# Performance work log

Measured on AMD Instinct MI355X. Metric: run time of the kernel, lower is better.

Reference implementation:

```python
import jax, jax.numpy as jnp
import numpy as np

EPS = 1e-4  # BatchNorm eps from module


def setup_inputs() -> dict:
    key = jax.random.key(0)
    ks = jax.random.split(key, 7)
    N, C, H, W = 4, 256, 64, 64
    D = C  # reduction=1
    x = jax.random.normal(ks[0], (N, C, H, W), dtype=jnp.float32)
    # 1x1 conv weights, msra-style scaled init
    s = 1.0 / np.sqrt(C)
    Wq = jax.random.normal(ks[1], (D, C), dtype=jnp.float32) * s
    Wk = jax.random.normal(ks[2], (D, C), dtype=jnp.float32) * s
    Wv = jax.random.normal(ks[3], (D, C), dtype=jnp.float32) * s
    Wo = jax.random.normal(ks[4], (C, D), dtype=jnp.float32) * s
    gamma = jnp.ones((C,), dtype=jnp.float32)
    beta = jnp.zeros((C,), dtype=jnp.float32)
    return {"x": x, "Wq": Wq, "Wk": Wk, "Wv": Wv, "Wo": Wo, "gamma": gamma, "beta": beta}


def reference(x, Wq, Wk, Wv, Wo, gamma, beta):
    N, C, H, W = x.shape
    D = Wq.shape[0]
    scale = 1.0 / jnp.sqrt(jnp.float32(D))
    xf = x.reshape(N, C, H * W)                      # (N, C, L)
    # 1x1 convs == per-position linear projections
    q = jnp.einsum('dc,ncl->nld', Wq, xf)            # (N, L, D)
    k = jnp.einsum('dc,ncl->nld', Wk, xf)            # (N, L, D)
    v = jnp.einsum('dc,ncl->nld', Wv, xf)            # (N, L, D)
    scores = jnp.einsum('nld,nmd->nlm', q, k) * scale  # (N, L, L)
    attn = jax.nn.softmax(scores, axis=2)
    out = jnp.einsum('nlm,nmd->nld', attn, v)        # (N, L, D)
    out = jnp.einsum('od,nld->nol', Wo, out).reshape(N, C, H, W)
    # BatchNorm2d (training-mode batch statistics, biased variance)
    mean = jnp.mean(out, axis=(0, 2, 3), keepdims=True)
    var = jnp.var(out, axis=(0, 2, 3), keepdims=True)
    out = (out - mean) * jax.lax.rsqrt(var + EPS)
    out = out * gamma[None, :, None, None] + beta[None, :, None, None]
    return x + out
```

## Files before the change

kernel.cpp:

```cpp
#include <hip/hip_runtime.h>
#include <cstdint>
#include <cstddef>

#define NB 4
#define CH 256
#define LL 4096

typedef unsigned short u16;
typedef unsigned int u32;
typedef unsigned char u8;
typedef __attribute__((ext_vector_type(8))) short bf16x8;
typedef __attribute__((ext_vector_type(4))) float f32x4;

#define GPTR(p) ((const __attribute__((address_space(1))) u32*)(p))
#define LPTR(p) ((__attribute__((address_space(3))) u32*)(p))

__device__ __forceinline__ float blo(u32 x) { return __uint_as_float(x << 16); }
__device__ __forceinline__ float bhi(u32 x) { return __uint_as_float(x & 0xffff0000u); }
__device__ __forceinline__ float b2f(u16 h) { return __uint_as_float(((u32)h) << 16); }
__device__ __forceinline__ u16 f2b(float f) {
    u32 u = __float_as_uint(f);
    u32 r = (u + 0x7fffu + ((u >> 16) & 1u)) >> 16;
    return (u16)r;
}
__device__ __forceinline__ u32 pack2(float a, float b) {
    return (u32)f2b(a) | ((u32)f2b(b) << 16);
}

__global__ __launch_bounds__(256) void castw_kernel(
    const float* __restrict__ Wq, const float* __restrict__ Wk,
    const float* __restrict__ Wv, const float* __restrict__ Wo,
    u16* __restrict__ Wb, float* __restrict__ stats) {
    const int i = blockIdx.x * 256 + threadIdx.x;
    const int m = blockIdx.y;
    if (m == 0 && blockIdx.x < 2) stats[i] = 0.0f;
    const float* src = (m == 0) ? Wq : (m == 1) ? Wk : (m == 2) ? Wv : Wo;
    float4 v = ((const float4*)src)[i];
    uint2 o;
    o.x = pack2(v.x, v.y);
    o.y = pack2(v.z, v.w);
    ((uint2*)(Wb + m * 65536))[i] = o;
}

__global__ __launch_bounds__(256) void tcast_kernel(
    const float* __restrict__ x, u16* __restrict__ xT) {
    const int n = blockIdx.z;
    const int c0 = blockIdx.y * 64, l0 = blockIdx.x * 64;
    __shared__ u16 t[64][72];
    const float* xs = x + (size_t)n * CH * LL;
    const int tid = threadIdx.x;
    const int lq = (tid & 15) * 4, cc = tid >> 4;
#pragma unroll
    for (int p = 0; p < 4; ++p) {
        int c = cc + p * 16;
        float4 v = *(const float4*)&xs[(size_t)(c0 + c) * LL + l0 + lq];
        t[lq + 0][c] = f2b(v.x);
        t[lq + 1][c] = f2b(v.y);
        t[lq + 2][c] = f2b(v.z);
        t[lq + 3][c] = f2b(v.w);
    }
    __syncthreads();
    u16* xo = xT + (size_t)n * LL * CH;
    const int l = tid >> 2, c8 = (tid & 3) * 16;
#pragma unroll
    for (int h = 0; h < 2; ++h) {
        uint4 vv = *(uint4*)&t[l][c8 + h * 8];
        *(uint4*)&xo[(size_t)(l0 + l) * CH + c0 + c8 + h * 8] = vv;
    }
}

__global__ __launch_bounds__(256, 2) void projqk_kernel(
    const u16* __restrict__ xT, const u16* __restrict__ Wb,
    u16* __restrict__ q, u16* __restrict__ k) {
    const int n = blockIdx.z;
    const int dhalf = blockIdx.y & 1, mat = blockIdx.y >> 1;
    const int l0 = blockIdx.x * 64;
    const int d0 = dhalf * 128;
    const int tid = threadIdx.x;
    const int w = tid >> 6, lane = tid & 63;
    const int lhi = lane >> 4, llo = lane & 15;

    __shared__ __align__(16) u16 Bs[128 * 256];

    const u16* xn = xT + (size_t)n * LL * CH;
    const u16* Wm = Wb + mat * 65536 + (size_t)d0 * CH;

#pragma unroll
    for (int i = 0; i < 16; ++i) {
        int s = i * 256 + tid;
        int r = s >> 5, c = s & 31;
        __builtin_amdgcn_global_load_lds(GPTR(Wm + r * CH + (c ^ (r & 31)) * 8),
                                         LPTR((char*)Bs + i * 4096 + w * 1024),
                                         16, 0, 0);
    }

    bf16x8 af[8];
    const u16* abase = xn + (size_t)(l0 + w * 16 + llo) * CH + lhi * 8;
#pragma unroll
    for (int ks = 0; ks < 8; ++ks) af[ks] = *(const bf16x8*)(abase + ks * 32);

    f32x4 acc[8];
#pragma unroll
    for (int t = 0; t < 8; ++t) acc[t] = (f32x4){0.f, 0.f, 0.f, 0.f};

    __syncthreads();

#pragma unroll
    for (int ks = 0; ks < 8; ++ks) {
#pragma unroll
        for (int ct = 0; ct < 8; ++ct) {
            const int rr = ct * 16 + llo;
            bf16x8 bf = *(const bf16x8*)(Bs + rr * CH +
                                         ((ks * 4 + lhi) ^ (rr & 31)) * 8);
            acc[ct] = __builtin_amdgcn_mfma_f32_16x16x32_bf16(af[ks], bf, acc[ct], 0, 0, 0);
        }
    }

    u16* o = (mat ? k : q) + (size_t)n * LL * CH;
#pragma unroll
    for (int r = 0; r < 4; ++r) {
        int lr = l0 + w * 16 + lhi * 4 + r;
#pragma unroll
        for (int ct = 0; ct < 8; ++ct)
            o[(size_t)lr * CH + d0 + ct * 16 + llo] = f2b(acc[ct][r]);
    }
}

__global__ __launch_bounds__(256, 2) void projv_kernel(
    const u16* __restrict__ xT, const u16* __restrict__ Wb,
    u16* __restrict__ vT) {
    const int n = blockIdx.z;
    const int d0 = blockIdx.y * 64;
    const int l0 = blockIdx.x * 128;
    const int tid = threadIdx.x;
    const int w = tid >> 6, lane = tid & 63;
    const int lhi = lane >> 4, llo = lane & 15;

    __shared__ __align__(16) u16 Bs[128 * 256];

    const u16* xn = xT + (size_t)n * LL * CH + (size_t)l0 * CH;
    const u16* Wm = Wb + 2 * 65536;

#pragma unroll
    for (int i = 0; i < 16; ++i) {
        int s = i * 256 + tid;
        int r = s >> 5, c = s & 31;
        __builtin_amdgcn_global_load_lds(GPTR(xn + r * CH + (c ^ (r & 31)) * 8),
                                         LPTR((char*)Bs + i * 4096 + w * 1024),
                                         16, 0, 0);
    }

    bf16x8 af[8];
    const u16* abase = Wm + (size_t)(d0 + w * 16 + llo) * CH + lhi * 8;
#pragma unroll
    for (int ks = 0; ks < 8; ++ks) af[ks] = *(const bf16x8*)(abase + ks * 32);

    f32x4 acc[8];
#pragma unroll
    for (int t = 0; t < 8; ++t) acc[t] = (f32x4){0.f, 0.f, 0.f, 0.f};

    __syncthreads();

#pragma unroll
    for (int ks = 0; ks < 8; ++ks) {
#pragma unroll
        for (int ct = 0; ct < 8; ++ct) {
            const int rr = ct * 16 + llo;
            bf16x8 bf = *(const bf16x8*)(Bs + rr * CH +
                                         ((ks * 4 + lhi) ^ (rr & 31)) * 8);
            acc[ct] = __builtin_amdgcn_mfma_f32_16x16x32_bf16(af[ks], bf, acc[ct], 0, 0, 0);
        }
    }

    u16* o = vT + (size_t)n * CH * LL;
#pragma unroll
    for (int r = 0; r < 4; ++r) {
        int dr = d0 + w * 16 + lhi * 4 + r;
#pragma unroll
        for (int ct = 0; ct < 8; ++ct)
            o[(size_t)dr * LL + l0 + ct * 16 + llo] = f2b(acc[ct][r]);
    }
}

__global__ __launch_bounds__(256, 2) void fattn_kernel(
    const u16* __restrict__ q, const u16* __restrict__ k,
    const u16* __restrict__ vT, u16* __restrict__ Op, float* __restrict__ l_s,
    int iters) {
    const int n = blockIdx.y;
    const int s_id = blockIdx.z;
    const int l0 = blockIdx.x * 128;
    const int m_base = s_id * iters * 32;
    const int tid = threadIdx.x;
    const int w = tid >> 6;
    const int lane = tid & 63;
    const int lhi = lane >> 4, llo = lane & 15;

    __shared__ __align__(16) char smem[65536];

    bf16x8 qf[2][8];
    {
        const u16* base = q + (size_t)(n * LL + l0 + w * 32 + llo) * CH + lhi * 8;
#pragma unroll
        for (int t = 0; t < 2; ++t)
#pragma unroll
            for (int ks = 0; ks < 8; ++ks)
                qf[t][ks] = *(const bf16x8*)(base + t * 16 * CH + ks * 32);
    }

    const u16* kg = k + (size_t)n * LL * CH;
    const u16* vg = vT + (size_t)n * CH * LL;

    int okK[4], okV[4];
#pragma unroll
    for (int i = 0; i < 4; ++i) {
        int s = i * 256 + tid;
        int rK = s >> 5;
        int cK = (s & 31) ^ rK;
        okK[i] = rK * CH + cK * 8;
        int dV = s >> 2;
        int cV = (s & 3) ^ ((dV & 3) ^ ((dV >> 2) & 3));
        okV[i] = dV * LL + cV * 8;
    }

    f32x4 oacc[2][16];
#pragma unroll
    for (int t = 0; t < 2; ++t)
#pragma unroll
        for (int ct = 0; ct < 16; ++ct) oacc[t][ct] = (f32x4){0.f, 0.f, 0.f, 0.f};
    float lrun[2] = {0.f, 0.f};

    const float C1 = 0.09016844005556021f;
    const int posV = (lhi ^ ((llo & 3) ^ (llo >> 2))) * 8;
    const int idxA = (llo + 32 * (lhi & 1)) * 4;
    const int idxB = idxA + 64;
    const bool selLo = (lhi < 2);

    {
        const u16* kg2 = kg + (size_t)m_base * CH;
        const u16* vg2 = vg + m_base;
#pragma unroll
        for (int i = 0; i < 4; ++i) {
            __builtin_amdgcn_global_load_lds(GPTR(kg2 + okK[i]),
                                             LPTR(smem + i * 4096 + w * 1024), 16, 0, 0);
            __builtin_amdgcn_global_load_lds(GPTR(vg2 + okV[i]),
                                             LPTR(smem + 32768 + i * 4096 + w * 1024),
                                             16, 0, 0);
        }
    }

    for (int it = 0; it < iters; ++it) {
        __syncthreads();
        if (it + 1 < iters) {
            const int m1 = m_base + (it + 1) * 32;
            const u16* kg2 = kg + (size_t)m1 * CH;
            const u16* vg2 = vg + m1;
            char* Kb = smem + ((it + 1) & 1) * 16384;
            char* Vb = smem + 32768 + ((it + 1) & 1) * 16384;
#pragma unroll
            for (int i = 0; i < 4; ++i) {
                __builtin_amdgcn_global_load_lds(GPTR(kg2 + okK[i]),
                                                 LPTR(Kb + i * 4096 + w * 1024), 16, 0, 0);
                __builtin_amdgcn_global_load_lds(GPTR(vg2 + okV[i]),
                                                 LPTR(Vb + i * 4096 + w * 1024), 16, 0, 0);
            }
        }
        const u16* Kl = (const u16*)(smem + (it & 1) * 16384);
        const u16* Vl = (const u16*)(smem + 32768 + (it & 1) * 16384);

        f32x4 s00 = (f32x4){0.f, 0.f, 0.f, 0.f};
        f32x4 s01 = (f32x4){0.f, 0.f, 0.f, 0.f};
        f32x4 s10 = (f32x4){0.f, 0.f, 0.f, 0.f};
        f32x4 s11 = (f32x4){0.f, 0.f, 0.f, 0.f};
#pragma unroll
        for (int ks = 0; ks < 8; ++ks) {
            const int cq = ks * 4 + lhi;
            bf16x8 b0 = *(const bf16x8*)(Kl + llo * 256 + (cq ^ llo) * 8);
            bf16x8 b1 = *(const bf16x8*)(Kl + (llo + 16) * 256 + (cq ^ (llo + 16)) * 8);
            s00 = __builtin_amdgcn_mfma_f32_16x16x32_bf16(b0, qf[0][ks], s00, 0, 0, 0);
            s10 = __builtin_amdgcn_mfma_f32_16x16x32_bf16(b0, qf[1][ks], s10, 0, 0, 0);
            s01 = __builtin_amdgcn_mfma_f32_16x16x32_bf16(b1, qf[0][ks], s01, 0, 0, 0);
            s11 = __builtin_amdgcn_mfma_f32_16x16x32_bf16(b1, qf[1][ks], s11, 0, 0, 0);
        }

        bf16x8 pa[2];
#pragma unroll
        for (int qt = 0; qt < 2; ++qt) {
            f32x4 sa = qt ? s10 : s00;
            f32x4 sb = qt ? s11 : s01;
            float pA0 = __builtin_amdgcn_exp2f(sa[0] * C1);
            float pA1 = __builtin_amdgcn_exp2f(sa[1] * C1);
            float pA2 = __builtin_amdgcn_exp2f(sa[2] * C1);
            float pA3 = __builtin_amdgcn_exp2f(sa[3] * C1);
            float pB0 = __builtin_amdgcn_exp2f(sb[0] * C1);
            float pB1 = __builtin_amdgcn_exp2f(sb[1] * C1);
            float pB2 = __builtin_amdgcn_exp2f(sb[2] * C1);
            float pB3 = __builtin_amdgcn_exp2f(sb[3] * C1);
            lrun[qt] += ((pA0 + pA1) + (pA2 + pA3)) + ((pB0 + pB1) + (pB2 + pB3));
            u32 w0, w1, w2, w3;
            asm("v_cvt_pk_bf16_f32 %0, %1, %2" : "=v"(w0) : "v"(pA0), "v"(pA1));
            asm("v_cvt_pk_bf16_f32 %0, %1, %2" : "=v"(w1) : "v"(pA2), "v"(pA3));
            asm("v_cvt_pk_bf16_f32 %0, %1, %2" : "=v"(w2) : "v"(pB0), "v"(pB1));
            asm("v_cvt_pk_bf16_f32 %0, %1, %2" : "=v"(w3) : "v"(pB2), "v"(pB3));
            int t0 = __builtin_amdgcn_ds_bpermute(idxA, (int)w0);
            int t2 = __builtin_amdgcn_ds_bpermute(idxA, (int)w2);
            int u0 = __builtin_amdgcn_ds_bpermute(idxA, (int)w1);
            int u2 = __builtin_amdgcn_ds_bpermute(idxA, (int)w3);
            int v0 = __builtin_amdgcn_ds_bpermute(idxB, (int)w0);
            int v2 = __builtin_amdgcn_ds_bpermute(idxB, (int)w2);
            int x0 = __builtin_amdgcn_ds_bpermute(idxB, (int)w1);
            int x2 = __builtin_amdgcn_ds_bpermute(idxB, (int)w3);
            union { u32 u[4]; bf16x8 v; } pk;
            pk.u[0] = selLo ? (u32)t0 : (u32)t2;
            pk.u[1] = selLo ? (u32)u0 : (u32)u2;
            pk.u[2] = selLo ? (u32)v0 : (u32)v2;
            pk.u[3] = selLo ? (u32)x0 : (u32)x2;
            pa[qt] = pk.v;
        }

#pragma unroll
        for (int ct = 0; ct < 16; ++ct) {
            bf16x8 vf = *(const bf16x8*)(Vl + (ct * 16 + llo) * 32 + posV);
            oacc[0][ct] = __builtin_amdgcn_mfma_f32_16x16x32_bf16(pa[0], vf, oacc[0][ct], 0, 0, 0);
            oacc[1][ct] = __builtin_amdgcn_mfma_f32_16x16x32_bf16(pa[1], vf, oacc[1][ct], 0, 0, 0);
        }
    }

    u16* ap = Op + (size_t)((s_id * NB + n) * (size_t)LL + l0 + w * 32) * CH;
    float* lp = l_s + (size_t)s_id * NB * LL + (size_t)n * LL + l0 + w * 32;
#pragma unroll
    for (int t = 0; t < 2; ++t) {
        float ls = lrun[t];
        ls += __shfl_xor(ls, 16);
        ls += __shfl_xor(ls, 32);
        if (lhi == 0) lp[t * 16 + llo] = ls;
#pragma unroll
        for (int r = 0; r < 4; ++r) {
            int lrow = t * 16 + lhi * 4 + r;
#pragma unroll
            for (int ct = 0; ct < 16; ++ct) {
                ap[(size_t)lrow * CH + ct * 16 + llo] = f2b(oacc[t][ct][r]);
            }
        }
    }
}

__global__ __launch_bounds__(256) void merge_kernel(
    const u16* __restrict__ Op, const float* __restrict__ l_s,
    u16* __restrict__ att, int S) {
    const size_t t8 = (size_t)blockIdx.x * 256 + threadIdx.x;
    const size_t flat = t8 * 8;
    const size_t row = flat >> 8;
    float lsum = 0.0f;
    for (int s = 0; s < S; ++s) lsum += l_s[(size_t)s * NB * LL + row];
    const float inv = 1.0f / lsum;
    float acc[8];
#pragma unroll
    for (int j = 0; j < 8; ++j) acc[j] = 0.0f;
    for (int s = 0; s < S; ++s) {
        uint4 raw = *(const uint4*)(Op + (size_t)s * NB * LL * CH + flat);
        acc[0] += blo(raw.x); acc[1] += bhi(raw.x);
        acc[2] += blo(raw.y); acc[3] += bhi(raw.y);
        acc[4] += blo(raw.z); acc[5] += bhi(raw.z);
        acc[6] += blo(raw.w); acc[7] += bhi(raw.w);
    }
    uint4 o;
    o.x = pack2(acc[0] * inv, acc[1] * inv);
    o.y = pack2(acc[2] * inv, acc[3] * inv);
    o.z = pack2(acc[4] * inv, acc[5] * inv);
    o.w = pack2(acc[6] * inv, acc[7] * inv);
    *(uint4*)(att + flat) = o;
}

__global__ __launch_bounds__(256, 2) void outm_kernel(
    const u16* __restrict__ Wb, const u16* __restrict__ att,
    u16* __restrict__ y, float* __restrict__ stats) {
    const int n = blockIdx.z;
    const int o0 = blockIdx.y * 64;
    const int l0 = blockIdx.x * 128;
    const int tid = threadIdx.x;
    const int w = tid >> 6, lane = tid & 63;
    const int lhi = lane >> 4, llo = lane & 15;

    __shared__ __align__(16) u16 Bs[128 * 256];

    const u16* an = att + (size_t)n * LL * CH + (size_t)l0 * CH;
    const u16* Wm = Wb + 3 * 65536;

#pragma unroll
    for (int i = 0; i < 16; ++i) {
        int s = i * 256 + tid;
        int r = s >> 5, c = s & 31;
        __builtin_amdgcn_global_load_lds(GPTR(an + r * CH + (c ^ (r & 31)) * 8),
                                         LPTR((char*)Bs + i * 4096 + w * 1024),
                                         16, 0, 0);
    }

    bf16x8 af[8];
    const u16* abase = Wm + (size_t)(o0 + w * 16 + llo) * CH + lhi * 8;
#pragma unroll
    for (int ks = 0; ks < 8; ++ks) af[ks] = *(const bf16x8*)(abase + ks * 32);

    f32x4 acc[8];
#pragma unroll
    for (int t = 0; t < 8; ++t) acc[t] = (f32x4){0.f, 0.f, 0.f, 0.f};

    __syncthreads();

#pragma unroll
    for (int ks = 0; ks < 8; ++ks) {
#pragma unroll
        for (int ct = 0; ct < 8; ++ct) {
            const int rr = ct * 16 + llo;
            bf16x8 bf = *(const bf16x8*)(Bs + rr * CH +
                                         ((ks * 4 + lhi) ^ (rr & 31)) * 8);
            acc[ct] = __builtin_amdgcn_mfma_f32_16x16x32_bf16(af[ks], bf, acc[ct], 0, 0, 0);
        }
    }

    u16* yn = y + (size_t)n * CH * LL;
#pragma unroll
    for (int r = 0; r < 4; ++r) {
        const int orow = o0 + w * 16 + lhi * 4 + r;
        float ts = 0.0f, tq = 0.0f;
#pragma unroll
        for (int ct = 0; ct < 8; ++ct) {
            float vv = acc[ct][r];
            yn[(size_t)orow * LL + l0 + ct * 16 + llo] = f2b(vv);
            ts += vv;
            tq += vv * vv;
        }
        ts += __shfl_xor(ts, 1); tq += __shfl_xor(tq, 1);
        ts += __shfl_xor(ts, 2); tq += __shfl_xor(tq, 2);
        ts += __shfl_xor(ts, 4); tq += __shfl_xor(tq, 4);
        ts += __shfl_xor(ts, 8); tq += __shfl_xor(tq, 8);
        if (llo == 0) {
            atomicAdd(&stats[orow], ts);
            atomicAdd(&stats[256 + orow], tq);
        }
    }
}

__global__ __launch_bounds__(256) void bn_kernel(
    const float* __restrict__ x, const u16* __restrict__ y,
    const float* __restrict__ stats, const float* __restrict__ gamma,
    const float* __restrict__ beta, float* __restrict__ out) {
    const int idx = blockIdx.x * 256 + threadIdx.x;
    const int base = idx * 4;
    const int c = (base >> 12) & 255;
    const float cnt = 1.0f / 16384.0f;
    float mean = stats[c] * cnt;
    float var = stats[256 + c] * cnt - mean * mean;
    float rstd = rsqrtf(var + 1e-4f);
    float g = gamma[c] * rstd;
    float b = beta[c];
    uint2 yv = ((const uint2*)y)[idx];
    float4 xv = ((const float4*)x)[idx];
    float4 o;
    o.x = xv.x + (blo(yv.x) - mean) * g + b;
    o.y = xv.y + (bhi(yv.x) - mean) * g + b;
    o.z = xv.z + (blo(yv.y) - mean) * g + b;
    o.w = xv.w + (bhi(yv.y) - mean) * g + b;
    ((float4*)out)[idx] = o;
}

extern "C" void kernel_launch(void* const* d_in, const int* in_sizes, int n_in,
                              void* d_out, int out_size, void* d_ws, size_t ws_size,
                              hipStream_t stream) {
    const float* x = (const float*)d_in[0];
    const float* Wq = (const float*)d_in[1];
    const float* Wk = (const float*)d_in[2];
    const float* Wv = (const float*)d_in[3];
    const float* Wo = (const float*)d_in[4];
    const float* gamma = (const float*)d_in[5];
    const float* beta = (const float*)d_in[6];
    float* out = (float*)d_out;

    const size_t elems = (size_t)NB * LL * CH;

    int S = 1;
    for (int cand = 4; cand >= 2; cand >>= 1) {
        size_t need = elems * 2 * (size_t)(3 + cand) +
                      (size_t)cand * NB * LL * 4 + 524288 + 8192;
        if (ws_size >= need) { S = cand; break; }
    }
    const int iters = 128 / S;

    char* wsb = (char*)d_ws;
    u16* q = (u16*)wsb;
    u16* k = q + elems;
    u16* vT = k + elems;
    u16* Op = vT + elems;
    u16* xT = Op;
    float* l_s = (float*)(Op + (size_t)S * elems);
    u16* Wb = (u16*)(l_s + (size_t)S * NB * LL);
    float* stats = (float*)(Wb + 4 * 65536);
    u16* att = q;
    u16* y = k;

    castw_kernel<<<dim3(64, 4), 256, 0, stream>>>(Wq, Wk, Wv, Wo, Wb, stats);
    tcast_kernel<<<dim3(LL / 64, CH / 64, NB), 256, 0, stream>>>(x, xT);
    projqk_kernel<<<dim3(LL / 64, 4, NB), 256, 0, stream>>>(xT, Wb, q, k);
    projv_kernel<<<dim3(LL / 128, CH / 64, NB), 256, 0, stream>>>(xT, Wb, vT);
    fattn_kernel<<<dim3(LL / 128, NB, S), 256, 0, stream>>>(q, k, vT, Op, l_s, iters);
    merge_kernel<<<(int)(elems / 8 / 256), 256, 0, stream>>>(Op, l_s, att, S);
    outm_kernel<<<dim3(LL / 128, CH / 64, NB), 256, 0, stream>>>(Wb, att, y, stats);
    bn_kernel<<<(NB * CH * LL / 4) / 256, 256, 0, stream>>>(x, y, stats, gamma, beta, out);
}
```

Baseline: 208.6 us.

## Software-pipeline PV matmul one iteration behind QK scores in attention loop

Restructures the attention inner loop so the P·V MFMA accumulation for the previous key block runs after the current block's QK^T scores. The exp/convert/permute of the current block then overlaps with the PV MFMAs. The V tile load now happens in the same iteration it is consumed, one iteration later, and a drained PV step is added after the loop with an extra barrier. This costs extra registers for the carried probabilities and relies on the barrier placement to keep the V double buffer consistent.

```diff
diff --git a/kernel.cpp b/kernel.cpp
--- a/kernel.cpp
+++ b/kernel.cpp
@@ -237,35 +237,36 @@
 
     {
         const u16* kg2 = kg + (size_t)m_base * CH;
-        const u16* vg2 = vg + m_base;
 #pragma unroll
         for (int i = 0; i < 4; ++i) {
             __builtin_amdgcn_global_load_lds(GPTR(kg2 + okK[i]),
                                              LPTR(smem + i * 4096 + w * 1024), 16, 0, 0);
-            __builtin_amdgcn_global_load_lds(GPTR(vg2 + okV[i]),
-                                             LPTR(smem + 32768 + i * 4096 + w * 1024),
-                                             16, 0, 0);
-        }
-    }
+        }
+    }
+
+    bf16x8 paP[2];
 
     for (int it = 0; it < iters; ++it) {
         __syncthreads();
         if (it + 1 < iters) {
-            const int m1 = m_base + (it + 1) * 32;
-            const u16* kg2 = kg + (size_t)m1 * CH;
-            const u16* vg2 = vg + m1;
+            const u16* kg2 = kg + (size_t)(m_base + (it + 1) * 32) * CH;
             char* Kb = smem + ((it + 1) & 1) * 16384;
-            char* Vb = smem + 32768 + ((it + 1) & 1) * 16384;
 #pragma unroll
             for (int i = 0; i < 4; ++i) {
                 __builtin_amdgcn_global_load_lds(GPTR(kg2 + okK[i]),
                                                  LPTR(Kb + i * 4096 + w * 1024), 16, 0, 0);
+            }
+        }
+        {
+            const u16* vg2 = vg + m_base + it * 32;
+            char* Vb = smem + 32768 + (it & 1) * 16384;
+#pragma unroll
+            for (int i = 0; i < 4; ++i) {
                 __builtin_amdgcn_global_load_lds(GPTR(vg2 + okV[i]),
                                                  LPTR(Vb + i * 4096 + w * 1024), 16, 0, 0);
             }
         }
         const u16* Kl = (const u16*)(smem + (it & 1) * 16384);
-        const u16* Vl = (const u16*)(smem + 32768 + (it & 1) * 16384);
 
         f32x4 s00 = (f32x4){0.f, 0.f, 0.f, 0.f};
         f32x4 s01 = (f32x4){0.f, 0.f, 0.f, 0.f};
@@ -282,7 +283,16 @@
             s11 = __builtin_amdgcn_mfma_f32_16x16x32_bf16(b1, qf[1][ks], s11, 0, 0, 0);
         }
 
-        bf16x8 pa[2];
+        if (it > 0) {
+            const u16* Vp = (const u16*)(smem + 32768 + ((it - 1) & 1) * 16384);
+#pragma unroll
+            for (int ct = 0; ct < 16; ++ct) {
+                bf16x8 vf = *(const bf16x8*)(Vp + (ct * 16 + llo) * 32 + posV);
+                oacc[0][ct] = __builtin_amdgcn_mfma_f32_16x16x32_bf16(paP[0], vf, oacc[0][ct], 0, 0, 0);
+                oacc[1][ct] = __builtin_amdgcn_mfma_f32_16x16x32_bf16(paP[1], vf, oacc[1][ct], 0, 0, 0);
+            }
+        }
+
 #pragma unroll
         for (int qt = 0; qt < 2; ++qt) {
             f32x4 sa = qt ? s10 : s00;
@@ -314,14 +324,18 @@
             pk.u[1] = selLo ? (u32)u0 : (u32)u2;
             pk.u[2] = selLo ? (u32)v0 : (u32)v2;
             pk.u[3] = selLo ? (u32)x0 : (u32)x2;
-            pa[qt] = pk.v;
-        }
-
+            paP[qt] = pk.v;
+        }
+    }
+
+    __syncthreads();
+    {
+        const u16* Vp = (const u16*)(smem + 32768 + ((iters - 1) & 1) * 16384);
 #pragma unroll
         for (int ct = 0; ct < 16; ++ct) {
-            bf16x8 vf = *(const bf16x8*)(Vl + (ct * 16 + llo) * 32 + posV);
-            oacc[0][ct] = __builtin_amdgcn_mfma_f32_16x16x32_bf16(pa[0], vf, oacc[0][ct], 0, 0, 0);
-            oacc[1][ct] = __builtin_amdgcn_mfma_f32_16x16x32_bf16(pa[1], vf, oacc[1][ct], 0, 0, 0);
+            bf16x8 vf = *(const bf16x8*)(Vp + (ct * 16 + llo) * 32 + posV);
+            oacc[0][ct] = __builtin_amdgcn_mfma_f32_16x16x32_bf16(paP[0], vf, oacc[0][ct], 0, 0, 0);
+            oacc[1][ct] = __builtin_amdgcn_mfma_f32_16x16x32_bf16(paP[1], vf, oacc[1][ct], 0, 0, 0);
         }
     }
 
```

Measured after the change: 218.8 us. 1.05x slower.

## Single-buffer V in attention for 3 blocks/CU and merge prep/projection launches

Applied to the files above, without the earlier changes.

The attention kernel keeps K double-buffered but holds V in a single shared buffer. The next V tile is loaded after the PV MFMAs, behind a barrier. This cuts LDS from 64 KB to 48 KB and raises launch bounds to 3 blocks per CU, aiming for higher occupancy. The cost is that V load latency is no longer hidden behind compute, and the tighter register budget may cause spills. Separately, the weight cast and x transpose-cast kernels are merged into one launch, and the QK and V projection kernels into another, to cut launch overhead.

```diff
diff --git a/kernel.cpp b/kernel.cpp
--- a/kernel.cpp
+++ b/kernel.cpp
@@ -27,162 +27,161 @@
     return (u32)f2b(a) | ((u32)f2b(b) << 16);
 }
 
-__global__ __launch_bounds__(256) void castw_kernel(
-    const float* __restrict__ Wq, const float* __restrict__ Wk,
-    const float* __restrict__ Wv, const float* __restrict__ Wo,
-    u16* __restrict__ Wb, float* __restrict__ stats) {
-    const int i = blockIdx.x * 256 + threadIdx.x;
-    const int m = blockIdx.y;
-    if (m == 0 && blockIdx.x < 2) stats[i] = 0.0f;
-    const float* src = (m == 0) ? Wq : (m == 1) ? Wk : (m == 2) ? Wv : Wo;
-    float4 v = ((const float4*)src)[i];
-    uint2 o;
-    o.x = pack2(v.x, v.y);
-    o.y = pack2(v.z, v.w);
-    ((uint2*)(Wb + m * 65536))[i] = o;
-}
-
-__global__ __launch_bounds__(256) void tcast_kernel(
-    const float* __restrict__ x, u16* __restrict__ xT) {
-    const int n = blockIdx.z;
-    const int c0 = blockIdx.y * 64, l0 = blockIdx.x * 64;
+__global__ __launch_bounds__(256) void prep_kernel(
+    const float* __restrict__ x, const float* __restrict__ Wq,
+    const float* __restrict__ Wk, const float* __restrict__ Wv,
+    const float* __restrict__ Wo, u16* __restrict__ Wb,
+    float* __restrict__ stats, u16* __restrict__ xT) {
+    const int id = blockIdx.x;
+    const int tid = threadIdx.x;
     __shared__ u16 t[64][72];
-    const float* xs = x + (size_t)n * CH * LL;
-    const int tid = threadIdx.x;
-    const int lq = (tid & 15) * 4, cc = tid >> 4;
-#pragma unroll
-    for (int p = 0; p < 4; ++p) {
-        int c = cc + p * 16;
-        float4 v = *(const float4*)&xs[(size_t)(c0 + c) * LL + l0 + lq];
-        t[lq + 0][c] = f2b(v.x);
-        t[lq + 1][c] = f2b(v.y);
-        t[lq + 2][c] = f2b(v.z);
-        t[lq + 3][c] = f2b(v.w);
-    }
-    __syncthreads();
-    u16* xo = xT + (size_t)n * LL * CH;
-    const int l = tid >> 2, c8 = (tid & 3) * 16;
-#pragma unroll
-    for (int h = 0; h < 2; ++h) {
-        uint4 vv = *(uint4*)&t[l][c8 + h * 8];
-        *(uint4*)&xo[(size_t)(l0 + l) * CH + c0 + c8 + h * 8] = vv;
-    }
-}
-
-__global__ __launch_bounds__(256, 2) void projqk_kernel(
+    if (id < 1024) {
+        const int n = id >> 8;
+        const int c0 = ((id >> 6) & 3) * 64, l0 = (id & 63) * 64;
+        const float* xs = x + (size_t)n * CH * LL;
+        const int lq = (tid & 15) * 4, cc = tid >> 4;
+#pragma unroll
+        for (int p = 0; p < 4; ++p) {
+            int c = cc + p * 16;
+            float4 v = *(const float4*)&xs[(size_t)(c0 + c) * LL + l0 + lq];
+            t[lq + 0][c] = f2b(v.x);
+            t[lq + 1][c] = f2b(v.y);
+            t[lq + 2][c] = f2b(v.z);
+            t[lq + 3][c] = f2b(v.w);
+        }
+        __syncthreads();
+        u16* xo = xT + (size_t)n * LL * CH;
+        const int l = tid >> 2, c8 = (tid & 3) * 16;
+#pragma unroll
+        for (int h = 0; h < 2; ++h) {
+            uint4 vv = *(uint4*)&t[l][c8 + h * 8];
+            *(uint4*)&xo[(size_t)(l0 + l) * CH + c0 + c8 + h * 8] = vv;
+        }
+    } else {
+        const int j = id - 1024;
+        const int i = (j & 63) * 256 + tid;
+        const int m = j >> 6;
+        if (m == 0 && (j & 63) < 2) stats[i] = 0.0f;
+        const float* src = (m == 0) ? Wq : (m == 1) ? Wk : (m == 2) ? Wv : Wo;
+        float4 v = ((const float4*)src)[i];
+        uint2 o;
+        o.x = pack2(v.x, v.y);
+        o.y = pack2(v.z, v.w);
+        ((uint2*)(Wb + m * 65536))[i] = o;
+    }
+}
+
+__global__ __launch_bounds__(256, 2) void proj_kernel(
     const u16* __restrict__ xT, const u16* __restrict__ Wb,
-    u16* __restrict__ q, u16* __restrict__ k) {
-    const int n = blockIdx.z;
-    const int dhalf = blockIdx.y & 1, mat = blockIdx.y >> 1;
-    const int l0 = blockIdx.x * 64;
-    const int d0 = dhalf * 128;
+    u16* __restrict__ q, u16* __restrict__ k, u16* __restrict__ vT) {
+    const int id = blockIdx.x;
     const int tid = threadIdx.x;
     const int w = tid >> 6, lane = tid & 63;
     const int lhi = lane >> 4, llo = lane & 15;
 
     __shared__ __align__(16) u16 Bs[128 * 256];
 
-    const u16* xn = xT + (size_t)n * LL * CH;
-    const u16* Wm = Wb + mat * 65536 + (size_t)d0 * CH;
-
-#pragma unroll
-    for (int i = 0; i < 16; ++i) {
-        int s = i * 256 + tid;
-        int r = s >> 5, c = s & 31;
-        __builtin_amdgcn_global_load_lds(GPTR(Wm + r * CH + (c ^ (r & 31)) * 8),
-                                         LPTR((char*)Bs + i * 4096 + w * 1024),
-                                         16, 0, 0);
-    }
-
-    bf16x8 af[8];
-    const u16* abase = xn + (size_t)(l0 + w * 16 + llo) * CH + lhi * 8;
-#pragma unroll
-    for (int ks = 0; ks < 8; ++ks) af[ks] = *(const bf16x8*)(abase + ks * 32);
-
-    f32x4 acc[8];
-#pragma unroll
-    for (int t = 0; t < 8; ++t) acc[t] = (f32x4){0.f, 0.f, 0.f, 0.f};
-
-    __syncthreads();
-
-#pragma unroll
-    for (int ks = 0; ks < 8; ++ks) {
-#pragma unroll
-        for (int ct = 0; ct < 8; ++ct) {
-            const int rr = ct * 16 + llo;
-            bf16x8 bf = *(const bf16x8*)(Bs + rr * CH +
-                                         ((ks * 4 + lhi) ^ (rr & 31)) * 8);
-            acc[ct] = __builtin_amdgcn_mfma_f32_16x16x32_bf16(af[ks], bf, acc[ct], 0, 0, 0);
-        }
-    }
-
-    u16* o = (mat ? k : q) + (size_t)n * LL * CH;
-#pragma unroll
-    for (int r = 0; r < 4; ++r) {
-        int lr = l0 + w * 16 + lhi * 4 + r;
-#pragma unroll
-        for (int ct = 0; ct < 8; ++ct)
-            o[(size_t)lr * CH + d0 + ct * 16 + llo] = f2b(acc[ct][r]);
-    }
-}
-
-__global__ __launch_bounds__(256, 2) void projv_kernel(
-    const u16* __restrict__ xT, const u16* __restrict__ Wb,
-    u16* __restrict__ vT) {
-    const int n = blockIdx.z;
-    const int d0 = blockIdx.y * 64;
-    const int l0 = blockIdx.x * 128;
-    const int tid = threadIdx.x;
-    const int w = tid >> 6, lane = tid & 63;
-    const int lhi = lane >> 4, llo = lane & 15;
-
-    __shared__ __align__(16) u16 Bs[128 * 256];
-
-    const u16* xn = xT + (size_t)n * LL * CH + (size_t)l0 * CH;
-    const u16* Wm = Wb + 2 * 65536;
-
-#pragma unroll
-    for (int i = 0; i < 16; ++i) {
-        int s = i * 256 + tid;
-        int r = s >> 5, c = s & 31;
-        __builtin_amdgcn_global_load_lds(GPTR(xn + r * CH + (c ^ (r & 31)) * 8),
-                                         LPTR((char*)Bs + i * 4096 + w * 1024),
-                                         16, 0, 0);
-    }
-
-    bf16x8 af[8];
-    const u16* abase = Wm + (size_t)(d0 + w * 16 + llo) * CH + lhi * 8;
-#pragma unroll
-    for (int ks = 0; ks < 8; ++ks) af[ks] = *(const bf16x8*)(abase + ks * 32);
-
-    f32x4 acc[8];
-#pragma unroll
-    for (int t = 0; t < 8; ++t) acc[t] = (f32x4){0.f, 0.f, 0.f, 0.f};
-
-    __syncthreads();
-
-#pragma unroll
-    for (int ks = 0; ks < 8; ++ks) {
-#pragma unroll
-        for (int ct = 0; ct < 8; ++ct) {
-            const int rr = ct * 16 + llo;
-            bf16x8 bf = *(const bf16x8*)(Bs + rr * CH +
-                                         ((ks * 4 + lhi) ^ (rr & 31)) * 8);
-            acc[ct] = __builtin_amdgcn_mfma_f32_16x16x32_bf16(af[ks], bf, acc[ct], 0, 0, 0);
-        }
-    }
-
-    u16* o = vT + (size_t)n * CH * LL;
-#pragma unroll
-    for (int r = 0; r < 4; ++r) {
-        int dr = d0 + w * 16 + lhi * 4 + r;
-#pragma unroll
-        for (int ct = 0; ct < 8; ++ct)
-            o[(size_t)dr * LL + l0 + ct * 16 + llo] = f2b(acc[ct][r]);
-    }
-}
-
-__global__ __launch_bounds__(256, 2) void fattn_kernel(
+    if (id < 1024) {
+        const int n = id >> 8;
+        const int yy = (id >> 6) & 3;
+        const int dhalf = yy & 1, mat = yy >> 1;
+        const int l0 = (id & 63) * 64;
+        const int d0 = dhalf * 128;
+
+        const u16* xn = xT + (size_t)n * LL * CH;
+        const u16* Wm = Wb + mat * 65536 + (size_t)d0 * CH;
+
+#pragma unroll
+        for (int i = 0; i < 16; ++i) {
+            int s = i * 256 + tid;
+            int r = s >> 5, c = s & 31;
+            __builtin_amdgcn_global_load_lds(GPTR(Wm + r * CH + (c ^ (r & 31)) * 8),
+                                             LPTR((char*)Bs + i * 4096 + w * 1024),
+                                             16, 0, 0);
+        }
+
+        bf16x8 af[8];
+        const u16* abase = xn + (size_t)(l0 + w * 16 + llo) * CH + lhi * 8;
+#pragma unroll
+        for (int ks = 0; ks < 8; ++ks) af[ks] = *(const bf16x8*)(abase + ks * 32);
+
+        f32x4 acc[8];
+#pragma unroll
+        for (int t = 0; t < 8; ++t) acc[t] = (f32x4){0.f, 0.f, 0.f, 0.f};
+
+        __syncthreads();
+
+#pragma unroll
+        for (int ks = 0; ks < 8; ++ks) {
+#pragma unroll
+            for (int ct = 0; ct < 8; ++ct) {
+                const int rr = ct * 16 + llo;
+                bf16x8 bf = *(const bf16x8*)(Bs + rr * CH +
+                                             ((ks * 4 + lhi) ^ (rr & 31)) * 8);
+                acc[ct] = __builtin_amdgcn_mfma_f32_16x16x32_bf16(af[ks], bf, acc[ct], 0, 0, 0);
+            }
+        }
+
+        u16* o = (mat ? k : q) + (size_t)n * LL * CH;
+#pragma unroll
+        for (int r = 0; r < 4; ++r) {
+            int lr = l0 + w * 16 + lhi * 4 + r;
+#pragma unroll
+            for (int ct = 0; ct < 8; ++ct)
+                o[(size_t)lr * CH + d0 + ct * 16 + llo] = f2b(acc[ct][r]);
+        }
+    } else {
+        const int j = id - 1024;
+        const int n = j >> 7;
+        const int d0 = ((j >> 5) & 3) * 64;
+        const int l0 = (j & 31) * 128;
+
+        const u16* xn = xT + (size_t)n * LL * CH + (size_t)l0 * CH;
+        const u16* Wm = Wb + 2 * 65536;
+
+#pragma unroll
+        for (int i = 0; i < 16; ++i) {
+            int s = i * 256 + tid;
+            int r = s >> 5, c = s & 31;
+            __builtin_amdgcn_global_load_lds(GPTR(xn + r * CH + (c ^ (r & 31)) * 8),
+                                             LPTR((char*)Bs + i * 4096 + w * 1024),
+                                             16, 0, 0);
+        }
+
+        bf16x8 af[8];
+        const u16* abase = Wm + (size_t)(d0 + w * 16 + llo) * CH + lhi * 8;
+#pragma unroll
+        for (int ks = 0; ks < 8; ++ks) af[ks] = *(const bf16x8*)(abase + ks * 32);
+
+        f32x4 acc[8];
+#pragma unroll
+        for (int t = 0; t < 8; ++t) acc[t] = (f32x4){0.f, 0.f, 0.f, 0.f};
+
+        __syncthreads();
+
+#pragma unroll
+        for (int ks = 0; ks < 8; ++ks) {
+#pragma unroll
+            for (int ct = 0; ct < 8; ++ct) {
+                const int rr = ct * 16 + llo;
+                bf16x8 bf = *(const bf16x8*)(Bs + rr * CH +
+                                             ((ks * 4 + lhi) ^ (rr & 31)) * 8);
+                acc[ct] = __builtin_amdgcn_mfma_f32_16x16x32_bf16(af[ks], bf, acc[ct], 0, 0, 0);
+            }
+        }
+
+        u16* o = vT + (size_t)n * CH * LL;
+#pragma unroll
+        for (int r = 0; r < 4; ++r) {
+            int dr = d0 + w * 16 + lhi * 4 + r;
+#pragma unroll
+            for (int ct = 0; ct < 8; ++ct)
+                o[(size_t)dr * LL + l0 + ct * 16 + llo] = f2b(acc[ct][r]);
+        }
+    }
+}
+
+__global__ __launch_bounds__(256, 3) void fattn_kernel(
     const u16* __restrict__ q, const u16* __restrict__ k,
     const u16* __restrict__ vT, u16* __restrict__ Op, float* __restrict__ l_s,
     int iters) {
@@ -195,7 +194,7 @@
     const int lane = tid & 63;
     const int lhi = lane >> 4, llo = lane & 15;
 
-    __shared__ __align__(16) char smem[65536];
+    __shared__ __align__(16) char smem[49152];
 
     bf16x8 qf[2][8];
     {
@@ -251,21 +250,16 @@
     for (int it = 0; it < iters; ++it) {
         __syncthreads();
         if (it + 1 < iters) {
-            const int m1 = m_base + (it + 1) * 32;
-            const u16* kg2 = kg + (size_t)m1 * CH;
-            const u16* vg2 = vg + m1;
+            const u16* kg2 = kg + (size_t)(m_base + (it + 1) * 32) * CH;
             char* Kb = smem + ((it + 1) & 1) * 16384;
-            char* Vb = smem + 32768 + ((it + 1) & 1) * 16384;
 #pragma unroll
             for (int i = 0; i < 4; ++i) {
                 __builtin_amdgcn_global_load_lds(GPTR(kg2 + okK[i]),
                                                  LPTR(Kb + i * 4096 + w * 1024), 16, 0, 0);
-                __builtin_amdgcn_global_load_lds(GPTR(vg2 + okV[i]),
-                                                 LPTR(Vb + i * 4096 + w * 1024), 16, 0, 0);
             }
         }
         const u16* Kl = (const u16*)(smem + (it & 1) * 16384);
-        const u16* Vl = (const u16*)(smem + 32768 + (it & 1) * 16384);
+        const u16* Vl = (const u16*)(smem + 32768);
 
         f32x4 s00 = (f32x4){0.f, 0.f, 0.f, 0.f};
         f32x4 s01 = (f32x4){0.f, 0.f, 0.f, 0.f};
@@ -323,6 +317,17 @@
             oacc[0][ct] = __builtin_amdgcn_mfma_f32_16x16x32_bf16(pa[0], vf, oacc[0][ct], 0, 0, 0);
             oacc[1][ct] = __builtin_amdgcn_mfma_f32_16x16x32_bf16(pa[1], vf, oacc[1][ct], 0, 0, 0);
         }
+
+        if (it + 1 < iters) {
+            __builtin_amdgcn_s_barrier();
+            const u16* vg2 = vg + m_base + (it + 1) * 32;
+#pragma unroll
+            for (int i = 0; i < 4; ++i) {
+                __builtin_amdgcn_global_load_lds(GPTR(vg2 + okV[i]),
+                                                 LPTR(smem + 32768 + i * 4096 + w * 1024),
+                                                 16, 0, 0);
+            }
+        }
     }
 
     u16* ap = Op + (size_t)((s_id * NB + n) * (size_t)LL + l0 + w * 32) * CH;
@@ -497,10 +502,8 @@
     u16* att = q;
     u16* y = k;
 
-    castw_kernel<<<dim3(64, 4), 256, 0, stream>>>(Wq, Wk, Wv, Wo, Wb, stats);
-    tcast_kernel<<<dim3(LL / 64, CH / 64, NB), 256, 0, stream>>>(x, xT);
-    projqk_kernel<<<dim3(LL / 64, 4, NB), 256, 0, stream>>>(xT, Wb, q, k);
-    projv_kernel<<<dim3(LL / 128, CH / 64, NB), 256, 0, stream>>>(xT, Wb, vT);
+    prep_kernel<<<1280, 256, 0, stream>>>(x, Wq, Wk, Wv, Wo, Wb, stats, xT);
+    proj_kernel<<<1536, 256, 0, stream>>>(xT, Wb, q, k, vT);
     fattn_kernel<<<dim3(LL / 128, NB, S), 256, 0, stream>>>(q, k, vT, Op, l_s, iters);
     merge_kernel<<<(int)(elems / 8 / 256), 256, 0, stream>>>(Op, l_s, att, S);
     outm_kernel<<<dim3(LL / 128, CH / 64, NB), 256, 0, stream>>>(Wb, att, y, stats);
```

Result: slower. 587.7 us (+181.7%).
